# Kernel optimization log

Measured on AMD Instinct MI355X. Metric: run time of the kernel, lower is better.

The kernel has to match this reference:

```python
import jax, jax.numpy as jnp
import numpy as np

N = 10000      # num nodes
E = 320000     # num edges
IN = 256       # in_dim
MP = 256       # mp_width
FL = 512       # fl_width
OUT = 64       # out_dim


def setup_inputs() -> dict:
    key = jax.random.key(0)
    ks = jax.random.split(key, 20)
    inp = {}
    inp["x"] = jax.random.normal(ks[0], (N, IN), dtype=jnp.float32)
    inp["edge_index"] = jax.random.randint(ks[1], (2, E), 0, N, dtype=jnp.int64)
    # iMP (frozen) linear layers: weight ~ N(0, 1) per nn.init.normal_(std=1.0)
    inp["mp_w0"] = jax.random.normal(ks[2], (IN, MP), dtype=jnp.float32)
    inp["mp_b0"] = jax.random.uniform(ks[3], (MP,), minval=-1.0, maxval=1.0) / np.sqrt(IN)
    inp["mp_w1"] = jax.random.normal(ks[4], (MP, MP), dtype=jnp.float32)
    inp["mp_b1"] = jax.random.uniform(ks[5], (MP,), minval=-1.0, maxval=1.0) / np.sqrt(MP)
    inp["mp_w2"] = jax.random.normal(ks[6], (MP, MP), dtype=jnp.float32)
    inp["mp_b2"] = jax.random.uniform(ks[7], (MP,), minval=-1.0, maxval=1.0) / np.sqrt(MP)
    # FC layers (torch default Linear init scale ~ 1/sqrt(fan_in))
    inp["fc_w0"] = jax.random.normal(ks[8], (MP, FL), dtype=jnp.float32) / np.sqrt(MP)
    inp["fc_b0"] = jnp.zeros((FL,), dtype=jnp.float32)
    inp["fc_w1"] = jax.random.normal(ks[9], (FL, FL), dtype=jnp.float32) / np.sqrt(FL)
    inp["fc_b1"] = jnp.zeros((FL,), dtype=jnp.float32)
    # injection projections
    inp["inj_w0"] = jax.random.normal(ks[10], (MP, FL), dtype=jnp.float32) / np.sqrt(MP)
    inp["inj_b0"] = jnp.zeros((FL,), dtype=jnp.float32)
    inp["inj_w1"] = jax.random.normal(ks[11], (MP, FL), dtype=jnp.float32) / np.sqrt(MP)
    inp["inj_b1"] = jnp.zeros((FL,), dtype=jnp.float32)
    inp["alpha"] = jnp.array(1.0, dtype=jnp.float32)
    inp["out_w"] = jax.random.normal(ks[12], (FL, OUT), dtype=jnp.float32) / np.sqrt(FL)
    inp["out_b"] = jnp.zeros((OUT,), dtype=jnp.float32)
    return inp


def _imp(x, w, b, row, col, deg_inv):
    # h = relu(W x); h /= deg; Ah = scatter_add over row of h[col]
    h = jax.nn.relu(x @ w + b) * deg_inv[:, None]      # [N, out]
    return jnp.zeros_like(h).at[row].add(h[col])       # gather + scatter-add


def reference(x, edge_index, mp_w0, mp_b0, mp_w1, mp_b1, mp_w2, mp_b2,
              fc_w0, fc_b0, fc_w1, fc_b1, inj_w0, inj_b0, inj_w1, inj_b1,
              alpha, out_w, out_b):
    row, col = edge_index[0], edge_index[1]
    deg = jax.ops.segment_sum(jnp.ones((E,), x.dtype), col, num_segments=N)
    # nodes with deg==0 never appear in col so clamping does not change output
    deg_inv = 1.0 / jnp.maximum(deg, 1.0)

    h = _imp(x, mp_w0, mp_b0, row, col, deg_inv)
    h = _imp(h, mp_w1, mp_b1, row, col, deg_inv)
    h = _imp(h, mp_w2, mp_b2, row, col, deg_inv)

    x_inject = h
    h = alpha * (jax.nn.relu(h) @ fc_w0 + fc_b0) + (x_inject @ inj_w0 + inj_b0)
    h = alpha * (jax.nn.relu(h) @ fc_w1 + fc_b1) + (x_inject @ inj_w1 + inj_b1)
    return h @ out_w + out_b
```

## Files before the change

### kernel.cpp

```cpp
#include <hip/hip_runtime.h>

#define N_NODES 10000
#define N_EDGES 320000
#define MPAD 10112
#define NBIN 10048
#define CHUNK 2048
#define NCH 157

typedef unsigned short u16;
typedef short bf16x8 __attribute__((ext_vector_type(8)));
typedef float f32x4 __attribute__((ext_vector_type(4)));

__device__ __forceinline__ u16 f2b(float f) {
  unsigned u = __builtin_bit_cast(unsigned, f);
  unsigned r = u + 0x7fffu + ((u >> 16) & 1u);
  return (u16)(r >> 16);
}
__device__ __forceinline__ unsigned pack2(float a, float b) {
  return (unsigned)f2b(a) | ((unsigned)f2b(b) << 16);
}
__device__ __forceinline__ float blo(unsigned u) { return __builtin_bit_cast(float, u << 16); }
__device__ __forceinline__ float bhi(unsigned u) { return __builtin_bit_cast(float, u & 0xffff0000u); }

__global__ void prep(
    const float* __restrict__ x,
    const float* __restrict__ w0, const float* __restrict__ w1, const float* __restrict__ w2,
    const float* __restrict__ fcw0, const float* __restrict__ injw0,
    const float* __restrict__ fcw1, const float* __restrict__ injw1,
    const float* __restrict__ outw,
    const float* __restrict__ fcb0, const float* __restrict__ injb0,
    const float* __restrict__ fcb1, const float* __restrict__ injb1,
    const float* __restrict__ alpha_p,
    u16* __restrict__ xb, u16* __restrict__ w0t, u16* __restrict__ w1t, u16* __restrict__ w2t,
    u16* __restrict__ wc1t, u16* __restrict__ wc2t, u16* __restrict__ owt,
    float* __restrict__ bias1, float* __restrict__ bias2)
{
  long i = (long)blockIdx.x * 256 + threadIdx.x;
  const float alpha = alpha_p[0];
  if (i < 640000L) {
    float4 v = ((const float4*)x)[i];
    uint2 o;
    o.x = pack2(v.x, v.y);
    o.y = pack2(v.z, v.w);
    *(uint2*)(xb + 4 * i) = o;
    return;
  }
  i -= 640000L;
  if (i < 65536) { w0t[i] = f2b(w0[(i & 255) * 256 + (i >> 8)]); return; }
  i -= 65536;
  if (i < 65536) { w1t[i] = f2b(w1[(i & 255) * 256 + (i >> 8)]); return; }
  i -= 65536;
  if (i < 65536) { w2t[i] = f2b(w2[(i & 255) * 256 + (i >> 8)]); return; }
  i -= 65536;
  if (i < 262144) {
    int n = (int)(i >> 9), k = (int)(i & 511);
    float v = (k < 256) ? alpha * fcw0[k * 512 + n] : injw0[(k - 256) * 512 + n];
    wc1t[i] = f2b(v); return;
  }
  i -= 262144;
  if (i < 393216) {
    int n = (int)(i / 768), k = (int)(i % 768);
    float v = (k < 512) ? alpha * fcw1[k * 512 + n] : injw1[(k - 512) * 512 + n];
    wc2t[i] = f2b(v); return;
  }
  i -= 393216;
  if (i < 32768) {
    int n = (int)(i >> 9), k = (int)(i & 511);
    owt[i] = f2b(outw[k * 64 + n]); return;
  }
  i -= 32768;
  if (i < 512) { bias1[i] = alpha * fcb0[i] + injb0[i]; return; }
  i -= 512;
  if (i < 512) { bias2[i] = alpha * fcb1[i] + injb1[i]; return; }
}

__global__ __launch_bounds__(256) void edge_hist(const int* __restrict__ ei,
                                                 int* __restrict__ histR,
                                                 int* __restrict__ histC) {
  __shared__ int hr[NBIN], hc[NBIN];
  const int ch = blockIdx.x, t = threadIdx.x;
  for (int i = t; i < NBIN; i += 256) { hr[i] = 0; hc[i] = 0; }
  __syncthreads();
  const int e0 = ch * CHUNK;
#pragma unroll
  for (int j = 0; j < CHUNK; j += 256) {
    int e = e0 + j + t;
    if (e < N_EDGES) {
      atomicAdd(&hr[ei[e]], 1);
      atomicAdd(&hc[ei[N_EDGES + e]], 1);
    }
  }
  __syncthreads();
  for (int i = t; i < NBIN; i += 256) {
    histR[(size_t)ch * NBIN + i] = hr[i];
    histC[(size_t)ch * NBIN + i] = hc[i];
  }
}

__global__ __launch_bounds__(256) void col_scan(const int* __restrict__ histR,
                                                const int* __restrict__ histC,
                                                int* __restrict__ chunkoff,
                                                int* __restrict__ cntR,
                                                float* __restrict__ deg_inv) {
  int r = blockIdx.x * 256 + threadIdx.x;
  if (r >= MPAD) return;
  if (r >= NBIN) { deg_inv[r] = 1.0f; return; }
  int run = 0, dg = 0;
#pragma unroll 4
  for (int ch = 0; ch < NCH; ++ch) {
    chunkoff[(size_t)ch * NBIN + r] = run;
    run += histR[(size_t)ch * NBIN + r];
    dg  += histC[(size_t)ch * NBIN + r];
  }
  cntR[r] = run;
  deg_inv[r] = 1.0f / (float)(dg > 1 ? dg : 1);
}

__global__ __launch_bounds__(1024) void row_scan(const int* __restrict__ cntR,
                                                 int* __restrict__ row_ptr) {
  const int t = threadIdx.x;
  const int i0 = t * 10;
  int v[10];
  int s = 0;
#pragma unroll
  for (int i = 0; i < 10; ++i) {
    int id = i0 + i;
    v[i] = (id < NBIN) ? cntR[id] : 0;
    s += v[i];
  }
  int lane = t & 63, wid = t >> 6;
  int incl = s;
#pragma unroll
  for (int off = 1; off < 64; off <<= 1) {
    int y = __shfl_up(incl, off, 64);
    if (lane >= off) incl += y;
  }
  __shared__ int wsum[16], wexc[16];
  if (lane == 63) wsum[wid] = incl;
  __syncthreads();
  if (t == 0) {
    int run = 0;
#pragma unroll
    for (int i = 0; i < 16; ++i) { wexc[i] = run; run += wsum[i]; }
  }
  __syncthreads();
  int run = wexc[wid] + incl - s;
#pragma unroll
  for (int i = 0; i < 10; ++i) {
    int id = i0 + i;
    if (id <= N_NODES) row_ptr[id] = run;
    run += v[i];
  }
}

__global__ __launch_bounds__(256) void place_edges(const int* __restrict__ ei,
                                                   const int* __restrict__ chunkoff,
                                                   const int* __restrict__ row_ptr,
                                                   int* __restrict__ csr) {
  __shared__ int cur[NBIN];
  const int ch = blockIdx.x, t = threadIdx.x;
  const int* co = chunkoff + (size_t)ch * NBIN;
  for (int i = t; i < NBIN; i += 256) cur[i] = co[i];
  __syncthreads();
  const int e0 = ch * CHUNK;
#pragma unroll
  for (int j = 0; j < CHUNK; j += 256) {
    int e = e0 + j + t;
    if (e < N_EDGES) {
      int r = ei[e];
      int c = ei[N_EDGES + e];
      int rank = atomicAdd(&cur[r], 1);
      csr[row_ptr[r] + rank] = c;
    }
  }
}

template<int K, bool RELU, bool SCALE, bool F32OUT>
__global__ __launch_bounds__(128) void gemm64(
    const u16* __restrict__ A, int lda,
    const u16* __restrict__ Bt,
    const float* __restrict__ bias,
    const float* __restrict__ scale,
    u16* __restrict__ Cb, float* __restrict__ Cf, int ldc)
{
  __shared__ u16 As[64 * 72];
  __shared__ u16 Bs[64 * 72];
  const int tid = threadIdx.x;
  const int m0 = blockIdx.x * 64;
  const int n0 = blockIdx.y * 64;
  const int wave = tid >> 6;
  const int lane = tid & 63;
  const int wr = wave * 32;
  const int lm = lane & 15;
  const int koff = (lane >> 4) * 8;

  const int srow = tid >> 2;
  const int scol = (tid & 3) * 16;
  const u16* Ag0 = A + (size_t)(m0 + srow) * lda + scol;
  const u16* Ag1 = A + (size_t)(m0 + srow + 32) * lda + scol;
  const u16* Bg0 = Bt + (size_t)(n0 + srow) * K + scol;
  const u16* Bg1 = Bt + (size_t)(n0 + srow + 32) * K + scol;
  u16* Asw0 = &As[srow * 72 + scol];
  u16* Asw1 = &As[(srow + 32) * 72 + scol];
  u16* Bsw0 = &Bs[srow * 72 + scol];
  u16* Bsw1 = &Bs[(srow + 32) * 72 + scol];

  f32x4 acc[2][4] = {};

  int4 pa0 = *(const int4*)(Ag0),     pa1 = *(const int4*)(Ag0 + 8);
  int4 pa2 = *(const int4*)(Ag1),     pa3 = *(const int4*)(Ag1 + 8);
  int4 pb0 = *(const int4*)(Bg0),     pb1 = *(const int4*)(Bg0 + 8);
  int4 pb2 = *(const int4*)(Bg1),     pb3 = *(const int4*)(Bg1 + 8);

#pragma unroll
  for (int kb = 0; kb < K; kb += 64) {
    __syncthreads();
    *(int4*)Asw0 = pa0; *(int4*)(Asw0 + 8) = pa1;
    *(int4*)Asw1 = pa2; *(int4*)(Asw1 + 8) = pa3;
    *(int4*)Bsw0 = pb0; *(int4*)(Bsw0 + 8) = pb1;
    *(int4*)Bsw1 = pb2; *(int4*)(Bsw1 + 8) = pb3;
    __syncthreads();
    if (kb + 64 < K) {
      pa0 = *(const int4*)(Ag0 + kb + 64); pa1 = *(const int4*)(Ag0 + kb + 72);
      pa2 = *(const int4*)(Ag1 + kb + 64); pa3 = *(const int4*)(Ag1 + kb + 72);
      pb0 = *(const int4*)(Bg0 + kb + 64); pb1 = *(const int4*)(Bg0 + kb + 72);
      pb2 = *(const int4*)(Bg1 + kb + 64); pb3 = *(const int4*)(Bg1 + kb + 72);
    }
#pragma unroll
    for (int ks = 0; ks < 2; ++ks) {
      bf16x8 af[2], bf[4];
#pragma unroll
      for (int mi = 0; mi < 2; ++mi)
        af[mi] = *(const bf16x8*)&As[(wr + mi * 16 + lm) * 72 + ks * 32 + koff];
#pragma unroll
      for (int ni = 0; ni < 4; ++ni)
        bf[ni] = *(const bf16x8*)&Bs[(ni * 16 + lm) * 72 + ks * 32 + koff];
#pragma unroll
      for (int mi = 0; mi < 2; ++mi)
#pragma unroll
        for (int ni = 0; ni < 4; ++ni)
          acc[mi][ni] = __builtin_amdgcn_mfma_f32_16x16x32_bf16(af[mi], bf[ni], acc[mi][ni], 0, 0, 0);
    }
  }

  const int q4 = (lane >> 4) * 4;
#pragma unroll
  for (int mi = 0; mi < 2; ++mi) {
#pragma unroll
    for (int ni = 0; ni < 4; ++ni) {
      const int gc = n0 + ni * 16 + lm;
      const float bv = bias[gc];
#pragma unroll
      for (int r = 0; r < 4; ++r) {
        const int gr = m0 + wr + mi * 16 + q4 + r;
        float v = acc[mi][ni][r] + bv;
        if (RELU) v = fmaxf(v, 0.f);
        if (SCALE) v *= scale[gr];
        if (F32OUT) {
          if (gr < N_NODES) Cf[(size_t)gr * ldc + gc] = v;
        } else {
          Cb[(size_t)gr * ldc + gc] = f2b(v);
        }
      }
    }
  }
}

__global__ __launch_bounds__(256) void aggregate(
    const u16* __restrict__ tmp, const int* __restrict__ row_ptr,
    const int* __restrict__ csr, u16* __restrict__ out0,
    u16* __restrict__ A1, u16* __restrict__ A2, int mode)
{
  const int wv = threadIdx.x >> 6;
  const int lane = threadIdx.x & 63;
  const int r = blockIdx.x * 4 + wv;
  const int half = lane >> 5;
  const int q = lane & 31;
  const int beg = row_ptr[r], end = row_ptr[r + 1];
  const size_t feat = (size_t)q * 16;
  const char* tb = (const char*)tmp;

  float s0 = 0.f, s1 = 0.f, s2 = 0.f, s3 = 0.f, s4 = 0.f, s5 = 0.f, s6 = 0.f, s7 = 0.f;
  int i = beg;
  for (; i + 8 <= end; i += 8) {
    uint4 v[4];
#pragma unroll
    for (int j = 0; j < 4; ++j)
      v[j] = *(const uint4*)(tb + (size_t)csr[i + 2 * j + half] * 512 + feat);
#pragma unroll
    for (int j = 0; j < 4; ++j) {
      s0 += blo(v[j].x); s1 += bhi(v[j].x); s2 += blo(v[j].y); s3 += bhi(v[j].y);
      s4 += blo(v[j].z); s5 += bhi(v[j].z); s6 += blo(v[j].w); s7 += bhi(v[j].w);
    }
  }
  for (; i < end; i += 2) {
    int id = i + half;
    if (id < end) {
      uint4 v = *(const uint4*)(tb + (size_t)csr[id] * 512 + feat);
      s0 += blo(v.x); s1 += bhi(v.x); s2 += blo(v.y); s3 += bhi(v.y);
      s4 += blo(v.z); s5 += bhi(v.z); s6 += blo(v.w); s7 += bhi(v.w);
    }
  }
  const int src = lane ^ 32;
  s0 += __shfl(s0, src, 64); s1 += __shfl(s1, src, 64);
  s2 += __shfl(s2, src, 64); s3 += __shfl(s3, src, 64);
  s4 += __shfl(s4, src, 64); s5 += __shfl(s5, src, 64);
  s6 += __shfl(s6, src, 64); s7 += __shfl(s7, src, 64);

  if (half == 0) {
    uint4 pv;
    pv.x = pack2(s0, s1); pv.y = pack2(s2, s3);
    pv.z = pack2(s4, s5); pv.w = pack2(s6, s7);
    if (mode == 0) {
      *(uint4*)((char*)out0 + (size_t)r * 512 + feat) = pv;
    } else {
      uint4 pr;
      pr.x = pack2(fmaxf(s0, 0.f), fmaxf(s1, 0.f));
      pr.y = pack2(fmaxf(s2, 0.f), fmaxf(s3, 0.f));
      pr.z = pack2(fmaxf(s4, 0.f), fmaxf(s5, 0.f));
      pr.w = pack2(fmaxf(s6, 0.f), fmaxf(s7, 0.f));
      *(uint4*)((char*)A1 + (size_t)r * 1024 + feat) = pr;
      *(uint4*)((char*)A1 + (size_t)r * 1024 + 512 + feat) = pv;
      *(uint4*)((char*)A2 + (size_t)r * 1536 + 1024 + feat) = pv;
    }
  }
}

extern "C" void kernel_launch(void* const* d_in, const int* in_sizes, int n_in,
                              void* d_out, int out_size, void* d_ws, size_t ws_size,
                              hipStream_t stream) {
  const float* x      = (const float*)d_in[0];
  const int*   ei     = (const int*)d_in[1];
  const float* mp_w0  = (const float*)d_in[2];
  const float* mp_b0  = (const float*)d_in[3];
  const float* mp_w1  = (const float*)d_in[4];
  const float* mp_b1  = (const float*)d_in[5];
  const float* mp_w2  = (const float*)d_in[6];
  const float* mp_b2  = (const float*)d_in[7];
  const float* fc_w0  = (const float*)d_in[8];
  const float* fc_b0  = (const float*)d_in[9];
  const float* fc_w1  = (const float*)d_in[10];
  const float* fc_b1  = (const float*)d_in[11];
  const float* inj_w0 = (const float*)d_in[12];
  const float* inj_b0 = (const float*)d_in[13];
  const float* inj_w1 = (const float*)d_in[14];
  const float* inj_b1 = (const float*)d_in[15];
  const float* alpha  = (const float*)d_in[16];
  const float* out_w  = (const float*)d_in[17];
  const float* out_b  = (const float*)d_in[18];
  float* out = (float*)d_out;

  char* p = (char*)d_ws;
  auto carve = [&](size_t bytes) -> void* {
    void* r = (void*)p;
    p += (bytes + 255) & ~(size_t)255;
    return r;
  };
  int*   histR    = (int*)carve((size_t)NCH * NBIN * 4);
  int*   histC    = (int*)carve((size_t)NCH * NBIN * 4);
  int*   chunkoff = (int*)carve((size_t)NCH * NBIN * 4);
  int*   cntR     = (int*)carve(NBIN * 4);
  int*   row_ptr  = (int*)carve((N_NODES + 1) * 4);
  int*   csr      = (int*)carve((size_t)N_EDGES * 4);
  float* deg_inv  = (float*)carve(MPAD * 4);
  float* bias1    = (float*)carve(512 * 4);
  float* bias2    = (float*)carve(512 * 4);
  u16* xb   = (u16*)carve((size_t)MPAD * 256 * 2);
  u16* w0t  = (u16*)carve(65536 * 2);
  u16* w1t  = (u16*)carve(65536 * 2);
  u16* w2t  = (u16*)carve(65536 * 2);
  u16* wc1t = (u16*)carve(262144 * 2);
  u16* wc2t = (u16*)carve(393216 * 2);
  u16* owt  = (u16*)carve(32768 * 2);
  u16* tmp  = (u16*)carve((size_t)MPAD * 256 * 2);
  u16* h    = (u16*)carve((size_t)MPAD * 256 * 2);
  u16* A1   = (u16*)carve((size_t)MPAD * 512 * 2);
  u16* A2   = (u16*)carve((size_t)MPAD * 768 * 2);
  u16* C2   = (u16*)carve((size_t)MPAD * 512 * 2);

  prep<<<5960, 256, 0, stream>>>(x, mp_w0, mp_w1, mp_w2, fc_w0, inj_w0, fc_w1, inj_w1,
                                 out_w, fc_b0, inj_b0, fc_b1, inj_b1, alpha,
                                 xb, w0t, w1t, w2t, wc1t, wc2t, owt, bias1, bias2);
  edge_hist<<<NCH, 256, 0, stream>>>(ei, histR, histC);
  col_scan<<<(MPAD + 255) / 256, 256, 0, stream>>>(histR, histC, chunkoff, cntR, deg_inv);
  row_scan<<<1, 1024, 0, stream>>>(cntR, row_ptr);
  place_edges<<<NCH, 256, 0, stream>>>(ei, chunkoff, row_ptr, csr);

  dim3 gmp(MPAD / 64, 4), gfc(MPAD / 64, 8), go(MPAD / 64, 1);
  gemm64<256, true, true, false><<<gmp, 128, 0, stream>>>(xb, 256, w0t, mp_b0, deg_inv, tmp, nullptr, 256);
  aggregate<<<2500, 256, 0, stream>>>(tmp, row_ptr, csr, h, nullptr, nullptr, 0);
  gemm64<256, true, true, false><<<gmp, 128, 0, stream>>>(h, 256, w1t, mp_b1, deg_inv, tmp, nullptr, 256);
  aggregate<<<2500, 256, 0, stream>>>(tmp, row_ptr, csr, h, nullptr, nullptr, 0);
  gemm64<256, true, true, false><<<gmp, 128, 0, stream>>>(h, 256, w2t, mp_b2, deg_inv, tmp, nullptr, 256);
  aggregate<<<2500, 256, 0, stream>>>(tmp, row_ptr, csr, nullptr, A1, A2, 1);
  gemm64<512, true, false, false><<<gfc, 128, 0, stream>>>(A1, 512, wc1t, bias1, nullptr, A2, nullptr, 768);
  gemm64<768, false, false, false><<<gfc, 128, 0, stream>>>(A2, 768, wc2t, bias2, nullptr, C2, nullptr, 512);
  gemm64<512, false, false, true><<<go, 128, 0, stream>>>(C2, 512, owt, out_b, nullptr, nullptr, out, 64);
}
```

Before: 267.9 us.

## Merge pipeline into two persistent cooperative kernels with grid syncs

Replaces the eleven separate launches (prep, histogram, scans, edge placement, GEMMs, aggregations) with two cooperative persistent kernels that loop over tiles and rows and use grid.sync between phases. This removes per-launch overhead and tail gaps between the small dependent kernels. In exchange, the grid is capped at occupancy times 256 blocks, so each phase has less parallelism and work per block is serialized through loops. Grid-wide barriers also cost time, and the row scan now runs in a single 256-thread block.

```diff
diff --git a/kernel.cpp b/kernel.cpp
--- a/kernel.cpp
+++ b/kernel.cpp
@@ -1,4 +1,7 @@
 #include <hip/hip_runtime.h>
+#include <hip/hip_cooperative_groups.h>
+
+namespace cg = cooperative_groups;
 
 #define N_NODES 10000
 #define N_EDGES 320000
@@ -6,6 +9,7 @@
 #define NBIN 10048
 #define CHUNK 2048
 #define NCH 157
+#define PREP_TOT 1525760L
 
 typedef unsigned short u16;
 typedef short bf16x8 __attribute__((ext_vector_type(8)));
@@ -22,334 +26,340 @@
 __device__ __forceinline__ float blo(unsigned u) { return __builtin_bit_cast(float, u << 16); }
 __device__ __forceinline__ float bhi(unsigned u) { return __builtin_bit_cast(float, u & 0xffff0000u); }
 
-__global__ void prep(
-    const float* __restrict__ x,
-    const float* __restrict__ w0, const float* __restrict__ w1, const float* __restrict__ w2,
-    const float* __restrict__ fcw0, const float* __restrict__ injw0,
-    const float* __restrict__ fcw1, const float* __restrict__ injw1,
-    const float* __restrict__ outw,
-    const float* __restrict__ fcb0, const float* __restrict__ injb0,
-    const float* __restrict__ fcb1, const float* __restrict__ injb1,
-    const float* __restrict__ alpha_p,
-    u16* __restrict__ xb, u16* __restrict__ w0t, u16* __restrict__ w1t, u16* __restrict__ w2t,
-    u16* __restrict__ wc1t, u16* __restrict__ wc2t, u16* __restrict__ owt,
-    float* __restrict__ bias1, float* __restrict__ bias2)
-{
-  long i = (long)blockIdx.x * 256 + threadIdx.x;
-  const float alpha = alpha_p[0];
+struct PP {
+  const float *x; const int *ei;
+  const float *w0, *w1, *w2, *fcw0, *injw0, *fcw1, *injw1, *outw;
+  const float *fcb0, *injb0, *fcb1, *injb1, *alpha;
+  u16 *xb, *w0t, *w1t, *w2t, *wc1t, *wc2t, *owt;
+  float *bias1, *bias2;
+  int *histR, *histC, *chunkoff, *cntR, *row_ptr, *csr;
+  float *deg_inv;
+};
+struct CP {
+  const u16 *xb, *w0t, *w1t, *w2t, *wc1t, *wc2t, *owt;
+  const float *mp_b0, *mp_b1, *mp_b2, *bias1, *bias2, *out_b, *deg_inv;
+  const int *row_ptr, *csr;
+  u16 *tmp, *h, *cat1, *cat2, *C2;
+  float *out;
+};
+
+__device__ void prep_item(long i, const PP& P, float alpha) {
   if (i < 640000L) {
-    float4 v = ((const float4*)x)[i];
+    float4 v = ((const float4*)P.x)[i];
     uint2 o;
     o.x = pack2(v.x, v.y);
     o.y = pack2(v.z, v.w);
-    *(uint2*)(xb + 4 * i) = o;
+    *(uint2*)(P.xb + 4 * i) = o;
     return;
   }
   i -= 640000L;
-  if (i < 65536) { w0t[i] = f2b(w0[(i & 255) * 256 + (i >> 8)]); return; }
+  if (i < 65536) { P.w0t[i] = f2b(P.w0[(i & 255) * 256 + (i >> 8)]); return; }
   i -= 65536;
-  if (i < 65536) { w1t[i] = f2b(w1[(i & 255) * 256 + (i >> 8)]); return; }
+  if (i < 65536) { P.w1t[i] = f2b(P.w1[(i & 255) * 256 + (i >> 8)]); return; }
   i -= 65536;
-  if (i < 65536) { w2t[i] = f2b(w2[(i & 255) * 256 + (i >> 8)]); return; }
+  if (i < 65536) { P.w2t[i] = f2b(P.w2[(i & 255) * 256 + (i >> 8)]); return; }
   i -= 65536;
   if (i < 262144) {
     int n = (int)(i >> 9), k = (int)(i & 511);
-    float v = (k < 256) ? alpha * fcw0[k * 512 + n] : injw0[(k - 256) * 512 + n];
-    wc1t[i] = f2b(v); return;
+    float v = (k < 256) ? alpha * P.fcw0[k * 512 + n] : P.injw0[(k - 256) * 512 + n];
+    P.wc1t[i] = f2b(v); return;
   }
   i -= 262144;
   if (i < 393216) {
     int n = (int)(i / 768), k = (int)(i % 768);
-    float v = (k < 512) ? alpha * fcw1[k * 512 + n] : injw1[(k - 512) * 512 + n];
-    wc2t[i] = f2b(v); return;
+    float v = (k < 512) ? alpha * P.fcw1[k * 512 + n] : P.injw1[(k - 512) * 512 + n];
+    P.wc2t[i] = f2b(v); return;
   }
   i -= 393216;
   if (i < 32768) {
     int n = (int)(i >> 9), k = (int)(i & 511);
-    owt[i] = f2b(outw[k * 64 + n]); return;
+    P.owt[i] = f2b(P.outw[k * 64 + n]); return;
   }
   i -= 32768;
-  if (i < 512) { bias1[i] = alpha * fcb0[i] + injb0[i]; return; }
+  if (i < 512) { P.bias1[i] = alpha * P.fcb0[i] + P.injb0[i]; return; }
   i -= 512;
-  if (i < 512) { bias2[i] = alpha * fcb1[i] + injb1[i]; return; }
-}
-
-__global__ __launch_bounds__(256) void edge_hist(const int* __restrict__ ei,
-                                                 int* __restrict__ histR,
-                                                 int* __restrict__ histC) {
-  __shared__ int hr[NBIN], hc[NBIN];
-  const int ch = blockIdx.x, t = threadIdx.x;
-  for (int i = t; i < NBIN; i += 256) { hr[i] = 0; hc[i] = 0; }
-  __syncthreads();
-  const int e0 = ch * CHUNK;
-#pragma unroll
-  for (int j = 0; j < CHUNK; j += 256) {
-    int e = e0 + j + t;
-    if (e < N_EDGES) {
-      atomicAdd(&hr[ei[e]], 1);
-      atomicAdd(&hc[ei[N_EDGES + e]], 1);
-    }
-  }
-  __syncthreads();
-  for (int i = t; i < NBIN; i += 256) {
-    histR[(size_t)ch * NBIN + i] = hr[i];
-    histC[(size_t)ch * NBIN + i] = hc[i];
-  }
-}
-
-__global__ __launch_bounds__(256) void col_scan(const int* __restrict__ histR,
-                                                const int* __restrict__ histC,
-                                                int* __restrict__ chunkoff,
-                                                int* __restrict__ cntR,
-                                                float* __restrict__ deg_inv) {
-  int r = blockIdx.x * 256 + threadIdx.x;
-  if (r >= MPAD) return;
-  if (r >= NBIN) { deg_inv[r] = 1.0f; return; }
-  int run = 0, dg = 0;
-#pragma unroll 4
-  for (int ch = 0; ch < NCH; ++ch) {
-    chunkoff[(size_t)ch * NBIN + r] = run;
-    run += histR[(size_t)ch * NBIN + r];
-    dg  += histC[(size_t)ch * NBIN + r];
-  }
-  cntR[r] = run;
-  deg_inv[r] = 1.0f / (float)(dg > 1 ? dg : 1);
-}
-
-__global__ __launch_bounds__(1024) void row_scan(const int* __restrict__ cntR,
-                                                 int* __restrict__ row_ptr) {
-  const int t = threadIdx.x;
-  const int i0 = t * 10;
-  int v[10];
-  int s = 0;
-#pragma unroll
-  for (int i = 0; i < 10; ++i) {
-    int id = i0 + i;
-    v[i] = (id < NBIN) ? cntR[id] : 0;
-    s += v[i];
-  }
-  int lane = t & 63, wid = t >> 6;
-  int incl = s;
-#pragma unroll
-  for (int off = 1; off < 64; off <<= 1) {
-    int y = __shfl_up(incl, off, 64);
-    if (lane >= off) incl += y;
-  }
-  __shared__ int wsum[16], wexc[16];
-  if (lane == 63) wsum[wid] = incl;
-  __syncthreads();
-  if (t == 0) {
-    int run = 0;
-#pragma unroll
-    for (int i = 0; i < 16; ++i) { wexc[i] = run; run += wsum[i]; }
-  }
-  __syncthreads();
-  int run = wexc[wid] + incl - s;
-#pragma unroll
-  for (int i = 0; i < 10; ++i) {
-    int id = i0 + i;
-    if (id <= N_NODES) row_ptr[id] = run;
-    run += v[i];
-  }
-}
-
-__global__ __launch_bounds__(256) void place_edges(const int* __restrict__ ei,
-                                                   const int* __restrict__ chunkoff,
-                                                   const int* __restrict__ row_ptr,
-                                                   int* __restrict__ csr) {
-  __shared__ int cur[NBIN];
-  const int ch = blockIdx.x, t = threadIdx.x;
-  const int* co = chunkoff + (size_t)ch * NBIN;
-  for (int i = t; i < NBIN; i += 256) cur[i] = co[i];
-  __syncthreads();
-  const int e0 = ch * CHUNK;
-#pragma unroll
-  for (int j = 0; j < CHUNK; j += 256) {
-    int e = e0 + j + t;
-    if (e < N_EDGES) {
-      int r = ei[e];
-      int c = ei[N_EDGES + e];
-      int rank = atomicAdd(&cur[r], 1);
-      csr[row_ptr[r] + rank] = c;
-    }
+  if (i < 512) { P.bias2[i] = alpha * P.fcb1[i] + P.injb1[i]; return; }
+}
+
+__global__ __launch_bounds__(256) void prolog(PP P) {
+  __shared__ int sh[2 * NBIN];
+  cg::grid_group grid = cg::this_grid();
+  const int tid = threadIdx.x, bid = blockIdx.x, nb = gridDim.x;
+
+  const float alpha = P.alpha[0];
+  for (long i = (long)bid * 256 + tid; i < PREP_TOT; i += (long)nb * 256)
+    prep_item(i, P, alpha);
+
+  for (int ch = bid; ch < NCH; ch += nb) {
+    for (int i = tid; i < 2 * NBIN; i += 256) sh[i] = 0;
+    __syncthreads();
+    const int e0 = ch * CHUNK;
+    for (int j = tid; j < CHUNK; j += 256) {
+      int e = e0 + j;
+      if (e < N_EDGES) {
+        atomicAdd(&sh[P.ei[e]], 1);
+        atomicAdd(&sh[NBIN + P.ei[N_EDGES + e]], 1);
+      }
+    }
+    __syncthreads();
+    for (int i = tid; i < NBIN; i += 256) {
+      P.histR[(size_t)ch * NBIN + i] = sh[i];
+      P.histC[(size_t)ch * NBIN + i] = sh[NBIN + i];
+    }
+    __syncthreads();
+  }
+  grid.sync();
+
+  for (int r = bid * 256 + tid; r < MPAD; r += nb * 256) {
+    if (r >= NBIN) { P.deg_inv[r] = 1.0f; continue; }
+    int run = 0, dg = 0;
+    for (int ch = 0; ch < NCH; ++ch) {
+      P.chunkoff[(size_t)ch * NBIN + r] = run;
+      run += P.histR[(size_t)ch * NBIN + r];
+      dg  += P.histC[(size_t)ch * NBIN + r];
+    }
+    P.cntR[r] = run;
+    P.deg_inv[r] = 1.0f / (float)(dg > 1 ? dg : 1);
+  }
+  grid.sync();
+
+  if (bid == 0) {
+    int v[40];
+    int s = 0;
+#pragma unroll
+    for (int i = 0; i < 40; ++i) {
+      int id = tid * 40 + i;
+      v[i] = (id < NBIN) ? P.cntR[id] : 0;
+      s += v[i];
+    }
+    int lane = tid & 63, wid = tid >> 6;
+    int incl = s;
+#pragma unroll
+    for (int off = 1; off < 64; off <<= 1) {
+      int y = __shfl_up(incl, off, 64);
+      if (lane >= off) incl += y;
+    }
+    if (lane == 63) sh[wid] = incl;
+    __syncthreads();
+    if (tid == 0) {
+      int run = 0;
+#pragma unroll
+      for (int i = 0; i < 4; ++i) { sh[4 + i] = run; run += sh[i]; }
+    }
+    __syncthreads();
+    int run = sh[4 + wid] + incl - s;
+#pragma unroll
+    for (int i = 0; i < 40; ++i) {
+      int id = tid * 40 + i;
+      if (id <= N_NODES) P.row_ptr[id] = run;
+      run += v[i];
+    }
+  }
+  grid.sync();
+
+  for (int ch = bid; ch < NCH; ch += nb) {
+    for (int i = tid; i < NBIN; i += 256) sh[i] = P.chunkoff[(size_t)ch * NBIN + i];
+    __syncthreads();
+    const int e0 = ch * CHUNK;
+    for (int j = tid; j < CHUNK; j += 256) {
+      int e = e0 + j;
+      if (e < N_EDGES) {
+        int r = P.ei[e];
+        int c = P.ei[N_EDGES + e];
+        int rank = atomicAdd(&sh[r], 1);
+        P.csr[P.row_ptr[r] + rank] = c;
+      }
+    }
+    __syncthreads();
   }
 }
 
 template<int K, bool RELU, bool SCALE, bool F32OUT>
-__global__ __launch_bounds__(128) void gemm64(
-    const u16* __restrict__ A, int lda,
-    const u16* __restrict__ Bt,
-    const float* __restrict__ bias,
-    const float* __restrict__ scale,
-    u16* __restrict__ Cb, float* __restrict__ Cf, int ldc)
-{
-  __shared__ u16 As[64 * 72];
-  __shared__ u16 Bs[64 * 72];
-  const int tid = threadIdx.x;
-  const int m0 = blockIdx.x * 64;
-  const int n0 = blockIdx.y * 64;
+__device__ void gemm_phase(int nTm, int nTn,
+                           const u16* __restrict__ A, int lda,
+                           const u16* __restrict__ Bt,
+                           const float* __restrict__ bias,
+                           const float* __restrict__ scale,
+                           u16* __restrict__ Cb, float* __restrict__ Cf, int ldc,
+                           u16* As, u16* Bs, int bid, int nb, int tid) {
   const int wave = tid >> 6;
   const int lane = tid & 63;
   const int wr = wave * 32;
   const int lm = lane & 15;
   const int koff = (lane >> 4) * 8;
-
   const int srow = tid >> 2;
   const int scol = (tid & 3) * 16;
-  const u16* Ag0 = A + (size_t)(m0 + srow) * lda + scol;
-  const u16* Ag1 = A + (size_t)(m0 + srow + 32) * lda + scol;
-  const u16* Bg0 = Bt + (size_t)(n0 + srow) * K + scol;
-  const u16* Bg1 = Bt + (size_t)(n0 + srow + 32) * K + scol;
-  u16* Asw0 = &As[srow * 72 + scol];
-  u16* Asw1 = &As[(srow + 32) * 72 + scol];
-  u16* Bsw0 = &Bs[srow * 72 + scol];
-  u16* Bsw1 = &Bs[(srow + 32) * 72 + scol];
-
-  f32x4 acc[2][4] = {};
-
-  int4 pa0 = *(const int4*)(Ag0),     pa1 = *(const int4*)(Ag0 + 8);
-  int4 pa2 = *(const int4*)(Ag1),     pa3 = *(const int4*)(Ag1 + 8);
-  int4 pb0 = *(const int4*)(Bg0),     pb1 = *(const int4*)(Bg0 + 8);
-  int4 pb2 = *(const int4*)(Bg1),     pb3 = *(const int4*)(Bg1 + 8);
-
-#pragma unroll
-  for (int kb = 0; kb < K; kb += 64) {
-    __syncthreads();
-    *(int4*)Asw0 = pa0; *(int4*)(Asw0 + 8) = pa1;
-    *(int4*)Asw1 = pa2; *(int4*)(Asw1 + 8) = pa3;
-    *(int4*)Bsw0 = pb0; *(int4*)(Bsw0 + 8) = pb1;
-    *(int4*)Bsw1 = pb2; *(int4*)(Bsw1 + 8) = pb3;
-    __syncthreads();
-    if (kb + 64 < K) {
-      pa0 = *(const int4*)(Ag0 + kb + 64); pa1 = *(const int4*)(Ag0 + kb + 72);
-      pa2 = *(const int4*)(Ag1 + kb + 64); pa3 = *(const int4*)(Ag1 + kb + 72);
-      pb0 = *(const int4*)(Bg0 + kb + 64); pb1 = *(const int4*)(Bg0 + kb + 72);
-      pb2 = *(const int4*)(Bg1 + kb + 64); pb3 = *(const int4*)(Bg1 + kb + 72);
-    }
-#pragma unroll
-    for (int ks = 0; ks < 2; ++ks) {
-      bf16x8 af[2], bf[4];
-#pragma unroll
-      for (int mi = 0; mi < 2; ++mi)
-        af[mi] = *(const bf16x8*)&As[(wr + mi * 16 + lm) * 72 + ks * 32 + koff];
-#pragma unroll
-      for (int ni = 0; ni < 4; ++ni)
-        bf[ni] = *(const bf16x8*)&Bs[(ni * 16 + lm) * 72 + ks * 32 + koff];
-#pragma unroll
-      for (int mi = 0; mi < 2; ++mi)
+  const int q4 = (lane >> 4) * 4;
+  const int nT = nTm * nTn;
+
+  for (int t = bid; t < nT; t += nb) {
+    const int m0 = (t % nTm) * 64;
+    const int n0 = (t / nTm) * 64;
+    const u16* Ag0 = A + (size_t)(m0 + srow) * lda + scol;
+    const u16* Ag1 = A + (size_t)(m0 + srow + 32) * lda + scol;
+    const u16* Bg0 = Bt + (size_t)(n0 + srow) * K + scol;
+    const u16* Bg1 = Bt + (size_t)(n0 + srow + 32) * K + scol;
+    u16* Asw0 = &As[srow * 72 + scol];
+    u16* Asw1 = &As[(srow + 32) * 72 + scol];
+    u16* Bsw0 = &Bs[srow * 72 + scol];
+    u16* Bsw1 = &Bs[(srow + 32) * 72 + scol];
+
+    f32x4 acc[2][4] = {};
+
+    int4 pa0 = *(const int4*)(Ag0), pa1 = *(const int4*)(Ag0 + 8);
+    int4 pa2 = *(const int4*)(Ag1), pa3 = *(const int4*)(Ag1 + 8);
+    int4 pb0 = *(const int4*)(Bg0), pb1 = *(const int4*)(Bg0 + 8);
+    int4 pb2 = *(const int4*)(Bg1), pb3 = *(const int4*)(Bg1 + 8);
+
+#pragma unroll
+    for (int kb = 0; kb < K; kb += 64) {
+      __syncthreads();
+      *(int4*)Asw0 = pa0; *(int4*)(Asw0 + 8) = pa1;
+      *(int4*)Asw1 = pa2; *(int4*)(Asw1 + 8) = pa3;
+      *(int4*)Bsw0 = pb0; *(int4*)(Bsw0 + 8) = pb1;
+      *(int4*)Bsw1 = pb2; *(int4*)(Bsw1 + 8) = pb3;
+      __syncthreads();
+      if (kb + 64 < K) {
+        pa0 = *(const int4*)(Ag0 + kb + 64); pa1 = *(const int4*)(Ag0 + kb + 72);
+        pa2 = *(const int4*)(Ag1 + kb + 64); pa3 = *(const int4*)(Ag1 + kb + 72);
+        pb0 = *(const int4*)(Bg0 + kb + 64); pb1 = *(const int4*)(Bg0 + kb + 72);
+        pb2 = *(const int4*)(Bg1 + kb + 64); pb3 = *(const int4*)(Bg1 + kb + 72);
+      }
+#pragma unroll
+      for (int ks = 0; ks < 2; ++ks) {
+        bf16x8 af[2], bf[4];
+#pragma unroll
+        for (int mi = 0; mi < 2; ++mi)
+          af[mi] = *(const bf16x8*)&As[(wr + mi * 16 + lm) * 72 + ks * 32 + koff];
 #pragma unroll
         for (int ni = 0; ni < 4; ++ni)
-          acc[mi][ni] = __builtin_amdgcn_mfma_f32_16x16x32_bf16(af[mi], bf[ni], acc[mi][ni], 0, 0, 0);
-    }
-  }
-
-  const int q4 = (lane >> 4) * 4;
-#pragma unroll
-  for (int mi = 0; mi < 2; ++mi) {
-#pragma unroll
-    for (int ni = 0; ni < 4; ++ni) {
-      const int gc = n0 + ni * 16 + lm;
-      const float bv = bias[gc];
-#pragma unroll
-      for (int r = 0; r < 4; ++r) {
-        const int gr = m0 + wr + mi * 16 + q4 + r;
-        float v = acc[mi][ni][r] + bv;
-        if (RELU) v = fmaxf(v, 0.f);
-        if (SCALE) v *= scale[gr];
-        if (F32OUT) {
-          if (gr < N_NODES) Cf[(size_t)gr * ldc + gc] = v;
-        } else {
-          Cb[(size_t)gr * ldc + gc] = f2b(v);
+          bf[ni] = *(const bf16x8*)&Bs[(ni * 16 + lm) * 72 + ks * 32 + koff];
+#pragma unroll
+        for (int mi = 0; mi < 2; ++mi)
+#pragma unroll
+          for (int ni = 0; ni < 4; ++ni)
+            acc[mi][ni] = __builtin_amdgcn_mfma_f32_16x16x32_bf16(af[mi], bf[ni], acc[mi][ni], 0, 0, 0);
+      }
+    }
+
+#pragma unroll
+    for (int mi = 0; mi < 2; ++mi) {
+#pragma unroll
+      for (int ni = 0; ni < 4; ++ni) {
+        const int gc = n0 + ni * 16 + lm;
+        const float bv = bias[gc];
+#pragma unroll
+        for (int r = 0; r < 4; ++r) {
+          const int gr = m0 + wr + mi * 16 + q4 + r;
+          float v = acc[mi][ni][r] + bv;
+          if (RELU) v = fmaxf(v, 0.f);
+          if (SCALE) v *= scale[gr];
+          if (F32OUT) {
+            if (gr < N_NODES) Cf[(size_t)gr * ldc + gc] = v;
+          } else {
+            Cb[(size_t)gr * ldc + gc] = f2b(v);
+          }
         }
       }
     }
-  }
-}
-
-__global__ __launch_bounds__(256) void aggregate(
-    const u16* __restrict__ tmp, const int* __restrict__ row_ptr,
-    const int* __restrict__ csr, u16* __restrict__ out0,
-    u16* __restrict__ A1, u16* __restrict__ A2, int mode)
-{
-  const int wv = threadIdx.x >> 6;
-  const int lane = threadIdx.x & 63;
-  const int r = blockIdx.x * 4 + wv;
+    __syncthreads();
+  }
+}
+
+__device__ void agg_phase(const u16* __restrict__ tmp, const int* __restrict__ row_ptr,
+                          const int* __restrict__ csr, u16* __restrict__ out0,
+                          u16* __restrict__ cat1, u16* __restrict__ cat2, int mode,
+                          int bid, int nb, int tid) {
+  const int wave = tid >> 6;
+  const int lane = tid & 63;
   const int half = lane >> 5;
   const int q = lane & 31;
-  const int beg = row_ptr[r], end = row_ptr[r + 1];
   const size_t feat = (size_t)q * 16;
   const char* tb = (const char*)tmp;
 
-  float s0 = 0.f, s1 = 0.f, s2 = 0.f, s3 = 0.f, s4 = 0.f, s5 = 0.f, s6 = 0.f, s7 = 0.f;
-  int i = beg;
-  for (; i + 8 <= end; i += 8) {
-    uint4 v[4];
-#pragma unroll
-    for (int j = 0; j < 4; ++j)
-      v[j] = *(const uint4*)(tb + (size_t)csr[i + 2 * j + half] * 512 + feat);
-#pragma unroll
-    for (int j = 0; j < 4; ++j) {
-      s0 += blo(v[j].x); s1 += bhi(v[j].x); s2 += blo(v[j].y); s3 += bhi(v[j].y);
-      s4 += blo(v[j].z); s5 += bhi(v[j].z); s6 += blo(v[j].w); s7 += bhi(v[j].w);
-    }
-  }
-  for (; i < end; i += 2) {
-    int id = i + half;
-    if (id < end) {
-      uint4 v = *(const uint4*)(tb + (size_t)csr[id] * 512 + feat);
-      s0 += blo(v.x); s1 += bhi(v.x); s2 += blo(v.y); s3 += bhi(v.y);
-      s4 += blo(v.z); s5 += bhi(v.z); s6 += blo(v.w); s7 += bhi(v.w);
-    }
-  }
-  const int src = lane ^ 32;
-  s0 += __shfl(s0, src, 64); s1 += __shfl(s1, src, 64);
-  s2 += __shfl(s2, src, 64); s3 += __shfl(s3, src, 64);
-  s4 += __shfl(s4, src, 64); s5 += __shfl(s5, src, 64);
-  s6 += __shfl(s6, src, 64); s7 += __shfl(s7, src, 64);
-
-  if (half == 0) {
-    uint4 pv;
-    pv.x = pack2(s0, s1); pv.y = pack2(s2, s3);
-    pv.z = pack2(s4, s5); pv.w = pack2(s6, s7);
-    if (mode == 0) {
-      *(uint4*)((char*)out0 + (size_t)r * 512 + feat) = pv;
-    } else {
-      uint4 pr;
-      pr.x = pack2(fmaxf(s0, 0.f), fmaxf(s1, 0.f));
-      pr.y = pack2(fmaxf(s2, 0.f), fmaxf(s3, 0.f));
-      pr.z = pack2(fmaxf(s4, 0.f), fmaxf(s5, 0.f));
-      pr.w = pack2(fmaxf(s6, 0.f), fmaxf(s7, 0.f));
-      *(uint4*)((char*)A1 + (size_t)r * 1024 + feat) = pr;
-      *(uint4*)((char*)A1 + (size_t)r * 1024 + 512 + feat) = pv;
-      *(uint4*)((char*)A2 + (size_t)r * 1536 + 1024 + feat) = pv;
-    }
-  }
+  for (int r = bid * 2 + wave; r < N_NODES; r += nb * 2) {
+    const int beg = row_ptr[r], end = row_ptr[r + 1];
+    float s0 = 0.f, s1 = 0.f, s2 = 0.f, s3 = 0.f, s4 = 0.f, s5 = 0.f, s6 = 0.f, s7 = 0.f;
+    int i = beg;
+    for (; i + 8 <= end; i += 8) {
+      uint4 v[4];
+#pragma unroll
+      for (int j = 0; j < 4; ++j)
+        v[j] = *(const uint4*)(tb + (size_t)csr[i + 2 * j + half] * 512 + feat);
+#pragma unroll
+      for (int j = 0; j < 4; ++j) {
+        s0 += blo(v[j].x); s1 += bhi(v[j].x); s2 += blo(v[j].y); s3 += bhi(v[j].y);
+        s4 += blo(v[j].z); s5 += bhi(v[j].z); s6 += blo(v[j].w); s7 += bhi(v[j].w);
+      }
+    }
+    for (; i < end; i += 2) {
+      int id = i + half;
+      if (id < end) {
+        uint4 v = *(const uint4*)(tb + (size_t)csr[id] * 512 + feat);
+        s0 += blo(v.x); s1 += bhi(v.x); s2 += blo(v.y); s3 += bhi(v.y);
+        s4 += blo(v.z); s5 += bhi(v.z); s6 += blo(v.w); s7 += bhi(v.w);
+      }
+    }
+    const int src = lane ^ 32;
+    s0 += __shfl(s0, src, 64); s1 += __shfl(s1, src, 64);
+    s2 += __shfl(s2, src, 64); s3 += __shfl(s3, src, 64);
+    s4 += __shfl(s4, src, 64); s5 += __shfl(s5, src, 64);
+    s6 += __shfl(s6, src, 64); s7 += __shfl(s7, src, 64);
+
+    if (half == 0) {
+      uint4 pv;
+      pv.x = pack2(s0, s1); pv.y = pack2(s2, s3);
+      pv.z = pack2(s4, s5); pv.w = pack2(s6, s7);
+      if (mode == 0) {
+        *(uint4*)((char*)out0 + (size_t)r * 512 + feat) = pv;
+      } else {
+        uint4 pr;
+        pr.x = pack2(fmaxf(s0, 0.f), fmaxf(s1, 0.f));
+        pr.y = pack2(fmaxf(s2, 0.f), fmaxf(s3, 0.f));
+        pr.z = pack2(fmaxf(s4, 0.f), fmaxf(s5, 0.f));
+        pr.w = pack2(fmaxf(s6, 0.f), fmaxf(s7, 0.f));
+        *(uint4*)((char*)cat1 + (size_t)r * 1024 + feat) = pr;
+        *(uint4*)((char*)cat1 + (size_t)r * 1024 + 512 + feat) = pv;
+        *(uint4*)((char*)cat2 + (size_t)r * 1536 + 1024 + feat) = pv;
+      }
+    }
+  }
+}
+
+__global__ __launch_bounds__(128) void compute(CP P) {
+  __shared__ u16 As[64 * 72];
+  __shared__ u16 Bs[64 * 72];
+  cg::grid_group grid = cg::this_grid();
+  const int tid = threadIdx.x, bid = blockIdx.x, nb = gridDim.x;
+
+  gemm_phase<256, true, true, false>(158, 4, P.xb, 256, P.w0t, P.mp_b0, P.deg_inv,
+                                     P.tmp, nullptr, 256, As, Bs, bid, nb, tid);
+  grid.sync();
+  agg_phase(P.tmp, P.row_ptr, P.csr, P.h, nullptr, nullptr, 0, bid, nb, tid);
+  grid.sync();
+  gemm_phase<256, true, true, false>(158, 4, P.h, 256, P.w1t, P.mp_b1, P.deg_inv,
+                                     P.tmp, nullptr, 256, As, Bs, bid, nb, tid);
+  grid.sync();
+  agg_phase(P.tmp, P.row_ptr, P.csr, P.h, nullptr, nullptr, 0, bid, nb, tid);
+  grid.sync();
+  gemm_phase<256, true, true, false>(158, 4, P.h, 256, P.w2t, P.mp_b2, P.deg_inv,
+                                     P.tmp, nullptr, 256, As, Bs, bid, nb, tid);
+  grid.sync();
+  agg_phase(P.tmp, P.row_ptr, P.csr, nullptr, P.cat1, P.cat2, 1, bid, nb, tid);
+  grid.sync();
+  gemm_phase<512, true, false, false>(158, 8, P.cat1, 512, P.wc1t, P.bias1, nullptr,
+                                      P.cat2, nullptr, 768, As, Bs, bid, nb, tid);
+  grid.sync();
+  gemm_phase<768, false, false, false>(158, 8, P.cat2, 768, P.wc2t, P.bias2, nullptr,
+                                       P.C2, nullptr, 512, As, Bs, bid, nb, tid);
+  grid.sync();
+  gemm_phase<512, false, false, true>(158, 1, P.C2, 512, P.owt, P.out_b, nullptr,
+                                      nullptr, P.out, 64, As, Bs, bid, nb, tid);
 }
 
 extern "C" void kernel_launch(void* const* d_in, const int* in_sizes, int n_in,
                               void* d_out, int out_size, void* d_ws, size_t ws_size,
                               hipStream_t stream) {
-  const float* x      = (const float*)d_in[0];
-  const int*   ei     = (const int*)d_in[1];
-  const float* mp_w0  = (const float*)d_in[2];
-  const float* mp_b0  = (const float*)d_in[3];
-  const float* mp_w1  = (const float*)d_in[4];
-  const float* mp_b1  = (const float*)d_in[5];
-  const float* mp_w2  = (const float*)d_in[6];
-  const float* mp_b2  = (const float*)d_in[7];
-  const float* fc_w0  = (const float*)d_in[8];
-  const float* fc_b0  = (const float*)d_in[9];
-  const float* fc_w1  = (const float*)d_in[10];
-  const float* fc_b1  = (const float*)d_in[11];
-  const float* inj_w0 = (const float*)d_in[12];
-  const float* inj_b0 = (const float*)d_in[13];
-  const float* inj_w1 = (const float*)d_in[14];
-  const float* inj_b1 = (const float*)d_in[15];
-  const float* alpha  = (const float*)d_in[16];
-  const float* out_w  = (const float*)d_in[17];
-  const float* out_b  = (const float*)d_in[18];
-  float* out = (float*)d_out;
-
   char* p = (char*)d_ws;
   auto carve = [&](size_t bytes) -> void* {
     void* r = (void*)p;
@@ -374,26 +384,55 @@
   u16* owt  = (u16*)carve(32768 * 2);
   u16* tmp  = (u16*)carve((size_t)MPAD * 256 * 2);
   u16* h    = (u16*)carve((size_t)MPAD * 256 * 2);
-  u16* A1   = (u16*)carve((size_t)MPAD * 512 * 2);
-  u16* A2   = (u16*)carve((size_t)MPAD * 768 * 2);
+  u16* cat1 = (u16*)carve((size_t)MPAD * 512 * 2);
+  u16* cat2 = (u16*)carve((size_t)MPAD * 768 * 2);
   u16* C2   = (u16*)carve((size_t)MPAD * 512 * 2);
 
-  prep<<<5960, 256, 0, stream>>>(x, mp_w0, mp_w1, mp_w2, fc_w0, inj_w0, fc_w1, inj_w1,
-                                 out_w, fc_b0, inj_b0, fc_b1, inj_b1, alpha,
-                                 xb, w0t, w1t, w2t, wc1t, wc2t, owt, bias1, bias2);
-  edge_hist<<<NCH, 256, 0, stream>>>(ei, histR, histC);
-  col_scan<<<(MPAD + 255) / 256, 256, 0, stream>>>(histR, histC, chunkoff, cntR, deg_inv);
-  row_scan<<<1, 1024, 0, stream>>>(cntR, row_ptr);
-  place_edges<<<NCH, 256, 0, stream>>>(ei, chunkoff, row_ptr, csr);
-
-  dim3 gmp(MPAD / 64, 4), gfc(MPAD / 64, 8), go(MPAD / 64, 1);
-  gemm64<256, true, true, false><<<gmp, 128, 0, stream>>>(xb, 256, w0t, mp_b0, deg_inv, tmp, nullptr, 256);
-  aggregate<<<2500, 256, 0, stream>>>(tmp, row_ptr, csr, h, nullptr, nullptr, 0);
-  gemm64<256, true, true, false><<<gmp, 128, 0, stream>>>(h, 256, w1t, mp_b1, deg_inv, tmp, nullptr, 256);
-  aggregate<<<2500, 256, 0, stream>>>(tmp, row_ptr, csr, h, nullptr, nullptr, 0);
-  gemm64<256, true, true, false><<<gmp, 128, 0, stream>>>(h, 256, w2t, mp_b2, deg_inv, tmp, nullptr, 256);
-  aggregate<<<2500, 256, 0, stream>>>(tmp, row_ptr, csr, nullptr, A1, A2, 1);
-  gemm64<512, true, false, false><<<gfc, 128, 0, stream>>>(A1, 512, wc1t, bias1, nullptr, A2, nullptr, 768);
-  gemm64<768, false, false, false><<<gfc, 128, 0, stream>>>(A2, 768, wc2t, bias2, nullptr, C2, nullptr, 512);
-  gemm64<512, false, false, true><<<go, 128, 0, stream>>>(C2, 512, owt, out_b, nullptr, nullptr, out, 64);
-}
+  PP pp;
+  pp.x = (const float*)d_in[0];
+  pp.ei = (const int*)d_in[1];
+  pp.w0 = (const float*)d_in[2];
+  pp.w1 = (const float*)d_in[4];
+  pp.w2 = (const float*)d_in[6];
+  pp.fcw0 = (const float*)d_in[8];
+  pp.fcw1 = (const float*)d_in[10];
+  pp.injw0 = (const float*)d_in[12];
+  pp.injw1 = (const float*)d_in[14];
+  pp.outw = (const float*)d_in[17];
+  pp.fcb0 = (const float*)d_in[9];
+  pp.injb0 = (const float*)d_in[13];
+  pp.fcb1 = (const float*)d_in[11];
+  pp.injb1 = (const float*)d_in[15];
+  pp.alpha = (const float*)d_in[16];
+  pp.xb = xb; pp.w0t = w0t; pp.w1t = w1t; pp.w2t = w2t;
+  pp.wc1t = wc1t; pp.wc2t = wc2t; pp.owt = owt;
+  pp.bias1 = bias1; pp.bias2 = bias2;
+  pp.histR = histR; pp.histC = histC; pp.chunkoff = chunkoff;
+  pp.cntR = cntR; pp.row_ptr = row_ptr; pp.csr = csr; pp.deg_inv = deg_inv;
+
+  CP cp;
+  cp.xb = xb; cp.w0t = w0t; cp.w1t = w1t; cp.w2t = w2t;
+  cp.wc1t = wc1t; cp.wc2t = wc2t; cp.owt = owt;
+  cp.mp_b0 = (const float*)d_in[3];
+  cp.mp_b1 = (const float*)d_in[5];
+  cp.mp_b2 = (const float*)d_in[7];
+  cp.bias1 = bias1; cp.bias2 = bias2;
+  cp.out_b = (const float*)d_in[18];
+  cp.deg_inv = deg_inv;
+  cp.row_ptr = row_ptr; cp.csr = csr;
+  cp.tmp = tmp; cp.h = h; cp.cat1 = cat1; cp.cat2 = cat2; cp.C2 = C2;
+  cp.out = (float*)d_out;
+
+  int occ1 = 0, occ2 = 0;
+  hipOccupancyMaxActiveBlocksPerMultiprocessor(&occ1, prolog, 256, 0);
+  hipOccupancyMaxActiveBlocksPerMultiprocessor(&occ2, compute, 128, 0);
+  if (occ1 < 1) occ1 = 1;
+  if (occ2 < 1) occ2 = 1;
+  int g1 = occ1 * 256;
+  int g2 = occ2 * 256;
+
+  void* a1[] = { &pp };
+  void* a2[] = { &cp };
+  hipLaunchCooperativeKernel((const void*)prolog, dim3(g1), dim3(256), a1, 0, stream);
+  hipLaunchCooperativeKernel((const void*)compute, dim3(g2), dim3(128), a2, 0, stream);
+}
```

After: 1.067 ms. +298.4%, slower.
